# Kernel optimization log

Measured on AMD Instinct MI355X. Metric: run time of the kernel, lower is better.

## Reference

```python
import jax, jax.numpy as jnp
import numpy as np

B, T, P, K, R, M = 32, 2048, 128, 256, 8, 64
TAU, TAU_X, TAU_Z = 5, 100.0, 100.0


def _mlp(x, layers):
    # torch nn.Linear: y = x @ W.T + b, each followed by tanh
    for W, b in layers:
        x = jnp.tanh(x @ W.T + b)
    return x


def setup_inputs() -> dict:
    key = jax.random.key(0)
    ks = jax.random.split(key, 24)
    g = lambda k, shp, s=0.1: (jax.random.normal(k, shp, dtype=jnp.float32) * s)
    inp = {
        "in_seq": jax.random.normal(ks[0], (B, T, P), dtype=jnp.float32),
        "L": g(ks[1], (K, R)),
        "Rm": g(ks[2], (K, R)),
        "Wz": g(ks[3], (M, M)),
        "Az_w": g(ks[4], (R, M)),
        "Az_b": jnp.zeros((R,), jnp.float32),
        "ex1_w": g(ks[5], (K, P)), "ex1_b": jnp.zeros((K,), jnp.float32),
        "ex2_w": g(ks[6], (K, K)), "ex2_b": jnp.zeros((K,), jnp.float32),
        "ex3_w": g(ks[7], (K, K)), "ex3_b": jnp.zeros((K,), jnp.float32),
        "ez1_w": g(ks[8], (M, P)), "ez1_b": jnp.zeros((M,), jnp.float32),
        "ez2_w": g(ks[9], (M, M)), "ez2_b": jnp.zeros((M,), jnp.float32),
        "ez3_w": g(ks[10], (M, M)), "ez3_b": jnp.zeros((M,), jnp.float32),
        "de1_w": g(ks[11], (K, K)), "de1_b": jnp.zeros((K,), jnp.float32),
        "de2_w": g(ks[12], (P, K)), "de2_b": jnp.zeros((P,), jnp.float32),
    }
    return inp


def reference(in_seq, L, Rm, Wz, Az_w, Az_b,
              ex1_w, ex1_b, ex2_w, ex2_b, ex3_w, ex3_b,
              ez1_w, ez1_b, ez2_w, ez2_b, ez3_w, ez3_b,
              de1_w, de1_b, de2_w, de2_b):
    enc_x = [(ex1_w, ex1_b), (ex2_w, ex2_b), (ex3_w, ex3_b)]
    enc_z = [(ez1_w, ez1_b), (ez2_w, ez2_b), (ez3_w, ez3_b)]
    dec = [(de1_w, de1_b), (de2_w, de2_b)]

    x_seq = _mlp(in_seq, enc_x)  # [B,T,K]
    z_seq = _mlp(in_seq, enc_z)  # [B,T,M]

    def step(carry, inp):
        x, z = carry          # [B,K], [B,M]
        t, xt, zt = inp       # scalar, [B,K], [B,M]
        # teacher forcing reset every TAU steps (not at t=0)
        reset = (t % TAU == 0) & (t > 0)
        x = jnp.where(reset, xt, x)
        z = jnp.where(reset, zt, z)
        # neuromodulator dynamics
        dz = -z + jnp.tanh(z) @ Wz.T
        z = z + dz / TAU_Z
        s = jax.nn.sigmoid(z @ Az_w.T + Az_b)  # [B,R]
        # low-rank recurrence: bmm(tanh(x), einsum('bir,jr,kr->bijk',s,L,R)[:,0])
        # == ((tanh(x) @ L) * s) @ R.T   (same math, O(K*R) per element)
        dx = -x + ((jnp.tanh(x) @ L) * s) @ Rm.T
        x = x + dx / TAU_X
        x_dec = _mlp(x, dec)  # [B,P]
        return (x, z), (x_dec, z)

    x0 = x_seq[:, 0, :]
    z0 = z_seq[:, 0, :]
    ts = jnp.arange(T)
    xs = jnp.swapaxes(x_seq, 0, 1)  # [T,B,K]
    zs = jnp.swapaxes(z_seq, 0, 1)  # [T,B,M]
    _, (x_pred_t, z_pred_t) = jax.lax.scan(step, (x0, z0), (ts, xs, zs))
    x_pred = jnp.swapaxes(x_pred_t, 0, 1)  # [B,T,P]
    z_pred = jnp.swapaxes(z_pred_t, 0, 1)  # [B,T,M]

    x_recon = _mlp(x_seq, dec)  # [B,T,P]
    return (x_pred, x_recon, z_pred, z_seq)
```

## Files before the change

kernel.cpp:

```cpp
#include <hip/hip_runtime.h>
#include <math.h>

constexpr int B = 32, T = 2048, P = 128, K = 256, R = 8, M = 64;
constexpr int BT = B * T;
constexpr int TAU = 5;
constexpr int NSEG = (T + TAU - 1) / TAU;
constexpr float INV_TAU_X = 1.0f / 100.0f;
constexpr float INV_TAU_Z = 1.0f / 100.0f;

typedef short bf16x4 __attribute__((ext_vector_type(4)));
typedef short bf16x8 __attribute__((ext_vector_type(8)));
typedef float f32x4 __attribute__((ext_vector_type(4)));

static __device__ __forceinline__ short f2bf(float f) {
  unsigned u = __builtin_bit_cast(unsigned, f);
  u += 0x7FFF + ((u >> 16) & 1);
  return (short)(u >> 16);
}
static __device__ __forceinline__ float bf2f(short h) {
  unsigned u = ((unsigned)(unsigned short)h) << 16;
  return __builtin_bit_cast(float, u);
}

static __device__ __forceinline__ float tanh_fast(float x) {
  const float e = __expf(2.f * x);
  return 1.f - 2.f * __builtin_amdgcn_rcpf(e + 1.f);
}
static __device__ __forceinline__ float sigmoid_fast(float x) {
  return __builtin_amdgcn_rcpf(1.f + __expf(-x));
}

template <int CTRL>
static __device__ __forceinline__ float dppadd(float p) {
  return p + __builtin_bit_cast(
                 float, __builtin_amdgcn_update_dpp(
                            0, __builtin_bit_cast(int, p), CTRL, 0xF, 0xF, true));
}

static __device__ __forceinline__ void allreduce8(float p[R]) {
#pragma unroll
  for (int r = 0; r < R; ++r) p[r] = dppadd<0xB1>(p[r]);
#pragma unroll
  for (int r = 0; r < R; ++r) p[r] = dppadd<0x4E>(p[r]);
#pragma unroll
  for (int r = 0; r < R; ++r) p[r] = dppadd<0x141>(p[r]);
#pragma unroll
  for (int r = 0; r < R; ++r) p[r] = dppadd<0x140>(p[r]);
#pragma unroll
  for (int r = 0; r < R; ++r)
    p[r] += __builtin_bit_cast(float, __builtin_amdgcn_ds_swizzle(
                                          __builtin_bit_cast(int, p[r]), 0x401F));
#pragma unroll
  for (int r = 0; r < R; ++r)
    p[r] += __shfl_xor(p[r], 32, 64);
}

struct W8 {
  const float* src[8];
  unsigned hoff[8];
  unsigned n4[8];
};
__global__ __launch_bounds__(256) void split8_kernel(W8 p, short* __restrict__ dst) {
  const int w = blockIdx.y;
  const int i = blockIdx.x * 256 + threadIdx.x;
  if (i >= (int)p.n4[w]) return;
  const float4 v = ((const float4*)p.src[w])[i];
  const float f[4] = {v.x, v.y, v.z, v.w};
  bf16x4 ph, pl;
#pragma unroll
  for (int q = 0; q < 4; ++q) {
    ph[q] = f2bf(f[q]);
    pl[q] = f2bf(f[q] - bf2f(ph[q]));
  }
  *(bf16x4*)&dst[p.hoff[w] + i * 4] = ph;
  *(bf16x4*)&dst[p.hoff[w] + p.n4[w] * 4 + i * 4] = pl;
}

struct FusedArgs {
  const float* A0;
  const short* Wh[5];
  const short* Wl[5];
  const float* bias[5];
  float* gout[5];
};

template <int I> struct Ly { static constexpr int v = I; };

template <int MAXW, int NL, int K0, int K1, int K2, int K3, int K4, int K5>
__global__ __launch_bounds__(512, 4) void fused_mlp(FusedArgs p) {
  constexpr int Kd[6] = {K0, K1, K2, K3, K4, K5};
  __shared__ short bufh[64 * MAXW];
  __shared__ short bufl[64 * MAXW];

  const int tid = threadIdx.x;
  const int wave = tid >> 6, lane = tid & 63;
  const int l16 = lane & 15, quad = lane >> 4;
  const int wm = wave >> 2, cg = wave & 3;
  const int row0 = blockIdx.x * 64;

  constexpr int G0 = K0 / 8;
  for (int u = tid; u < 64 * G0; u += 512) {
    const int row = u / G0, g = u % G0;
    const float* gp = p.A0 + (size_t)(row0 + row) * K0 + g * 8;
    const f32x4 v0 = *(const f32x4*)gp;
    const f32x4 v1 = *(const f32x4*)(gp + 4);
    bf16x8 ph, pl;
#pragma unroll
    for (int e = 0; e < 4; ++e) {
      ph[e] = f2bf(v0[e]);
      pl[e] = f2bf(v0[e] - bf2f(ph[e]));
      ph[4 + e] = f2bf(v1[e]);
      pl[4 + e] = f2bf(v1[e] - bf2f(ph[4 + e]));
    }
    const int off = ((g >> 3) * 64 + row) * 64 + (((g & 7) ^ (row & 7)) * 8);
    *(bf16x8*)&bufh[off] = ph;
    *(bf16x8*)&bufl[off] = pl;
  }
  __syncthreads();

  auto do_layer = [&](auto lc) {
    constexpr int l = decltype(lc)::v;
    constexpr int KIN = Kd[l], KOUT = Kd[l + 1];
    constexpr int JT = KOUT / 64;
    constexpr int NT64 = KIN / 64;
    const int cols0w = cg * (KOUT / 4);

    f32x4 acc[2][JT];
#pragma unroll
    for (int i = 0; i < 2; ++i)
#pragma unroll
      for (int j = 0; j < JT; ++j) acc[i][j] = (f32x4){0.f, 0.f, 0.f, 0.f};

#pragma unroll
    for (int kt = 0; kt < NT64; ++kt) {
#pragma unroll
      for (int kk = 0; kk < 2; ++kk) {
        const int qc = kk * 4 + quad;
        bf16x8 bh[JT], bl[JT];
#pragma unroll
        for (int j = 0; j < JT; ++j) {
          const size_t boff = (size_t)(cols0w + j * 16 + l16) * KIN +
                              kt * 64 + kk * 32 + quad * 8;
          bh[j] = *(const bf16x8*)(p.Wh[l] + boff);
          bl[j] = *(const bf16x8*)(p.Wl[l] + boff);
        }
        bf16x8 ah[2], al[2];
#pragma unroll
        for (int i = 0; i < 2; ++i) {
          const int r = wm * 32 + i * 16 + l16;
          const int off = (kt * 64 + r) * 64 + ((qc ^ (r & 7)) * 8);
          ah[i] = *(const bf16x8*)&bufh[off];
          al[i] = *(const bf16x8*)&bufl[off];
        }
#pragma unroll
        for (int j = 0; j < JT; ++j)
#pragma unroll
          for (int i = 0; i < 2; ++i) {
            acc[i][j] = __builtin_amdgcn_mfma_f32_16x16x32_bf16(
                ah[i], bh[j], acc[i][j], 0, 0, 0);
            acc[i][j] = __builtin_amdgcn_mfma_f32_16x16x32_bf16(
                al[i], bh[j], acc[i][j], 0, 0, 0);
            acc[i][j] = __builtin_amdgcn_mfma_f32_16x16x32_bf16(
                ah[i], bl[j], acc[i][j], 0, 0, 0);
          }
      }
    }
    if constexpr (l < NL - 1) __syncthreads();

    float* gout = p.gout[l];
#pragma unroll
    for (int j = 0; j < JT; ++j) {
      const int col = cols0w + j * 16 + l16;
      const float bj = p.bias[l][col];
#pragma unroll
      for (int i = 0; i < 2; ++i) {
#pragma unroll
        for (int r = 0; r < 4; ++r) {
          const float v = tanh_fast(acc[i][j][r] + bj);
          const int row = wm * 32 + i * 16 + quad * 4 + r;
          if constexpr (l < NL - 1) {
            const int off = ((col >> 6) * 64 + row) * 64 +
                            ((((col & 63) >> 3) ^ (row & 7)) * 8) + (col & 7);
            const short h = f2bf(v);
            bufh[off] = h;
            bufl[off] = f2bf(v - bf2f(h));
          }
          if (gout) gout[(size_t)(row0 + row) * KOUT + col] = v;
        }
      }
    }
    if constexpr (l < NL - 1) __syncthreads();
  };

  do_layer(Ly<0>{});
  if constexpr (NL > 1) do_layer(Ly<1>{});
  if constexpr (NL > 2) do_layer(Ly<2>{});
  if constexpr (NL > 3) do_layer(Ly<3>{});
  if constexpr (NL > 4) do_layer(Ly<4>{});
}

__global__ __launch_bounds__(512) void scan_kernel(
    float* xs,
    const float* __restrict__ z_seq,
    const float* __restrict__ Lm, const float* __restrict__ Rm,
    const float* __restrict__ Wz, const float* __restrict__ Az_w,
    const float* __restrict__ Az_b,
    float* __restrict__ z_pred) {
  __shared__ __align__(16) float Wz_s[M][68];
  __shared__ __align__(16) float Ls[K * R];
  __shared__ __align__(16) float Rs[K * R];
  __shared__ __align__(16) float tz_s[8][M];

  const int tid = threadIdx.x;
  for (int i = tid; i < M * M; i += 512) Wz_s[i >> 6][i & 63] = Wz[i];
  ((float4*)Ls)[tid] = ((const float4*)Lm)[tid];
  ((float4*)Rs)[tid] = ((const float4*)Rm)[tid];
  __syncthreads();

  const int wave = tid >> 6;
  const int lane = tid & 63;
  const int chain = blockIdx.x * 8 + wave;
  const int b = chain / NSEG;
  const int seg = chain % NSEG;
  const int t0 = seg * TAU;

  float azw[R], azb[R];
#pragma unroll
  for (int r = 0; r < R; ++r) {
    azw[r] = Az_w[r * M + lane];
    azb[r] = Az_b[r];
  }

  float x[4], z;
  {
    const size_t base = ((size_t)b * T + t0);
#pragma unroll
    for (int j = 0; j < 4; ++j) x[j] = xs[base * K + lane + 64 * j];
    z = z_seq[base * M + lane];
  }

  const float4* wrow = (const float4*)&Wz_s[lane][0];
  const float4* trow = (const float4*)&tz_s[wave][0];

  for (int tt = 0; tt < TAU; ++tt) {
    const int t = t0 + tt;
    const float tz = tanh_fast(z);
    tz_s[wave][lane] = tz;
    float zacc = 0.f;
#pragma unroll
    for (int j = 0; j < 16; ++j) {
      const float4 w = wrow[j], tv = trow[j];
      zacc += w.x * tv.x + w.y * tv.y + w.z * tv.z + w.w * tv.w;
    }
    const float znew = z + (zacc - z) * INV_TAU_Z;

    float s[R];
#pragma unroll
    for (int r = 0; r < R; ++r) s[r] = znew * azw[r];
    allreduce8(s);
#pragma unroll
    for (int r = 0; r < R; ++r) s[r] = sigmoid_fast(s[r] + azb[r]);

    float tx4[4];
#pragma unroll
    for (int j = 0; j < 4; ++j) tx4[j] = tanh_fast(x[j]);
    float v[R];
#pragma unroll
    for (int r = 0; r < R; ++r) v[r] = 0.f;
#pragma unroll
    for (int j = 0; j < 4; ++j) {
      const int kb = (lane + 64 * j) * 8;
      const f32x4 la = *(const f32x4*)&Ls[kb];
      const f32x4 lb = *(const f32x4*)&Ls[kb + 4];
      const float txj = tx4[j];
      v[0] += txj * la[0]; v[1] += txj * la[1];
      v[2] += txj * la[2]; v[3] += txj * la[3];
      v[4] += txj * lb[0]; v[5] += txj * lb[1];
      v[6] += txj * lb[2]; v[7] += txj * lb[3];
    }
    allreduce8(v);
#pragma unroll
    for (int r = 0; r < R; ++r) v[r] *= s[r];
#pragma unroll
    for (int j = 0; j < 4; ++j) {
      const int kb = (lane + 64 * j) * 8;
      const f32x4 ra = *(const f32x4*)&Rs[kb];
      const f32x4 rb = *(const f32x4*)&Rs[kb + 4];
      const float xacc = v[0] * ra[0] + v[1] * ra[1] + v[2] * ra[2] +
                         v[3] * ra[3] + v[4] * rb[0] + v[5] * rb[1] +
                         v[6] * rb[2] + v[7] * rb[3];
      x[j] = x[j] + (xacc - x[j]) * INV_TAU_X;
    }

    if (t < T) {
      const size_t o = ((size_t)b * T + t);
#pragma unroll
      for (int j = 0; j < 4; ++j) xs[o * K + lane + 64 * j] = x[j];
      z_pred[o * M + lane] = znew;
    }
    z = znew;
  }
}

extern "C" void kernel_launch(void* const* d_in, const int* in_sizes, int n_in,
                              void* d_out, int out_size, void* d_ws,
                              size_t ws_size, hipStream_t stream) {
  const float* in_seq = (const float*)d_in[0];
  const float* Lm    = (const float*)d_in[1];
  const float* Rm    = (const float*)d_in[2];
  const float* Wz    = (const float*)d_in[3];
  const float* Az_w  = (const float*)d_in[4];
  const float* Az_b  = (const float*)d_in[5];
  const float* ex1_w = (const float*)d_in[6];
  const float* ex1_b = (const float*)d_in[7];
  const float* ex2_w = (const float*)d_in[8];
  const float* ex2_b = (const float*)d_in[9];
  const float* ex3_w = (const float*)d_in[10];
  const float* ex3_b = (const float*)d_in[11];
  const float* ez1_w = (const float*)d_in[12];
  const float* ez1_b = (const float*)d_in[13];
  const float* ez2_w = (const float*)d_in[14];
  const float* ez2_b = (const float*)d_in[15];
  const float* ez3_w = (const float*)d_in[16];
  const float* ez3_b = (const float*)d_in[17];
  const float* de1_w = (const float*)d_in[18];
  const float* de1_b = (const float*)d_in[19];
  const float* de2_w = (const float*)d_in[20];
  const float* de2_b = (const float*)d_in[21];

  float* out = (float*)d_out;
  float* x_pred  = out;
  float* x_recon = out + (size_t)BT * P;
  float* z_pred  = out + (size_t)2 * BT * P;
  float* z_seq   = out + (size_t)2 * BT * P + (size_t)BT * M;

  float* X0 = (float*)d_ws;
  short* Wr = (short*)(X0 + (size_t)BT * K);

  const unsigned HO_EX1 = 0,      HO_EX2 = 65536,  HO_EX3 = 196608;
  const unsigned HO_DE1 = 327680, HO_DE2 = 458752;
  const unsigned HO_EZ1 = 524288, HO_EZ2 = 540672, HO_EZ3 = 548864;

  W8 w8;
  w8.src[0] = ex1_w; w8.hoff[0] = HO_EX1; w8.n4[0] = 8192;
  w8.src[1] = ex2_w; w8.hoff[1] = HO_EX2; w8.n4[1] = 16384;
  w8.src[2] = ex3_w; w8.hoff[2] = HO_EX3; w8.n4[2] = 16384;
  w8.src[3] = de1_w; w8.hoff[3] = HO_DE1; w8.n4[3] = 16384;
  w8.src[4] = de2_w; w8.hoff[4] = HO_DE2; w8.n4[4] = 8192;
  w8.src[5] = ez1_w; w8.hoff[5] = HO_EZ1; w8.n4[5] = 2048;
  w8.src[6] = ez2_w; w8.hoff[6] = HO_EZ2; w8.n4[6] = 1024;
  w8.src[7] = ez3_w; w8.hoff[7] = HO_EZ3; w8.n4[7] = 1024;
  split8_kernel<<<dim3(64, 8), dim3(256), 0, stream>>>(w8, Wr);

  const dim3 fgrid(BT / 64), fblk(512);

  {
    FusedArgs a{};
    a.A0 = in_seq;
    a.Wh[0] = Wr + HO_EX1; a.Wl[0] = Wr + HO_EX1 + 32768; a.bias[0] = ex1_b;
    a.Wh[1] = Wr + HO_EX2; a.Wl[1] = Wr + HO_EX2 + 65536; a.bias[1] = ex2_b;
    a.Wh[2] = Wr + HO_EX3; a.Wl[2] = Wr + HO_EX3 + 65536; a.bias[2] = ex3_b;
    a.Wh[3] = Wr + HO_DE1; a.Wl[3] = Wr + HO_DE1 + 65536; a.bias[3] = de1_b;
    a.Wh[4] = Wr + HO_DE2; a.Wl[4] = Wr + HO_DE2 + 32768; a.bias[4] = de2_b;
    a.gout[2] = X0;
    a.gout[4] = x_recon;
    fused_mlp<256, 5, 128, 256, 256, 256, 256, 128>
        <<<fgrid, fblk, 0, stream>>>(a);
  }
  {
    FusedArgs a{};
    a.A0 = in_seq;
    a.Wh[0] = Wr + HO_EZ1; a.Wl[0] = Wr + HO_EZ1 + 8192; a.bias[0] = ez1_b;
    a.Wh[1] = Wr + HO_EZ2; a.Wl[1] = Wr + HO_EZ2 + 4096; a.bias[1] = ez2_b;
    a.Wh[2] = Wr + HO_EZ3; a.Wl[2] = Wr + HO_EZ3 + 4096; a.bias[2] = ez3_b;
    a.gout[2] = z_seq;
    fused_mlp<128, 3, 128, 64, 64, 64, 0, 0><<<fgrid, fblk, 0, stream>>>(a);
  }
  scan_kernel<<<dim3(B * NSEG / 8), dim3(512), 0, stream>>>(
      X0, z_seq, Lm, Rm, Wz, Az_w, Az_b, z_pred);
  {
    FusedArgs a{};
    a.A0 = X0;
    a.Wh[0] = Wr + HO_DE1; a.Wl[0] = Wr + HO_DE1 + 65536; a.bias[0] = de1_b;
    a.Wh[1] = Wr + HO_DE2; a.Wl[1] = Wr + HO_DE2 + 32768; a.bias[1] = de2_b;
    a.gout[1] = x_pred;
    fused_mlp<256, 2, 256, 256, 128, 0, 0, 0><<<fgrid, fblk, 0, stream>>>(a);
  }
}
```

Measured before the change: 618.8 us.

## Reshape fused MLP wave tiling per layer and prefetch weight fragments three deep

The fused MLP kernel now picks its wave layout per layer: 8 column groups by 1 row group when the output width is at least 128, otherwise 4 by 2. Each wave then owns more rows (up to 64) or fewer columns, which changes how much each global weight fragment is reused. Weight fragments also go into a three-slot register ring that is loaded two k-phases ahead of use, so global-load latency is hidden behind the MFMAs. The cost is more register pressure, since the ring and the larger accumulator sets may cause spills under launch_bounds(512,4), and narrow layers get less column parallelism.

```diff
diff --git a/kernel.cpp b/kernel.cpp
--- a/kernel.cpp
+++ b/kernel.cpp
@@ -95,7 +95,6 @@
   const int tid = threadIdx.x;
   const int wave = tid >> 6, lane = tid & 63;
   const int l16 = lane & 15, quad = lane >> 4;
-  const int wm = wave >> 2, cg = wave & 3;
   const int row0 = blockIdx.x * 64;
 
   constexpr int G0 = K0 / 8;
@@ -121,49 +120,59 @@
   auto do_layer = [&](auto lc) {
     constexpr int l = decltype(lc)::v;
     constexpr int KIN = Kd[l], KOUT = Kd[l + 1];
-    constexpr int JT = KOUT / 64;
-    constexpr int NT64 = KIN / 64;
-    const int cols0w = cg * (KOUT / 4);
-
-    f32x4 acc[2][JT];
-#pragma unroll
-    for (int i = 0; i < 2; ++i)
+    constexpr int NWN = (KOUT >= 128) ? 8 : 4;
+    constexpr int NWM = 8 / NWN;
+    constexpr int NI = 4 / NWM;
+    constexpr int JT = KOUT / (NWN * 16);
+    constexpr int NPH = KIN / 32;
+    const int wm = wave / NWN, cg = wave % NWN;
+    const int cols0w = cg * (KOUT / NWN);
+    const int rbase = wm * NI * 16;
+
+    f32x4 acc[NI][JT];
+#pragma unroll
+    for (int i = 0; i < NI; ++i)
 #pragma unroll
       for (int j = 0; j < JT; ++j) acc[i][j] = (f32x4){0.f, 0.f, 0.f, 0.f};
 
-#pragma unroll
-    for (int kt = 0; kt < NT64; ++kt) {
-#pragma unroll
-      for (int kk = 0; kk < 2; ++kk) {
-        const int qc = kk * 4 + quad;
-        bf16x8 bh[JT], bl[JT];
-#pragma unroll
-        for (int j = 0; j < JT; ++j) {
-          const size_t boff = (size_t)(cols0w + j * 16 + l16) * KIN +
-                              kt * 64 + kk * 32 + quad * 8;
-          bh[j] = *(const bf16x8*)(p.Wh[l] + boff);
-          bl[j] = *(const bf16x8*)(p.Wl[l] + boff);
+    bf16x8 bh[3][JT], bl[3][JT];
+    auto loadB = [&](int ph, int slot) {
+#pragma unroll
+      for (int j = 0; j < JT; ++j) {
+        const size_t boff =
+            (size_t)(cols0w + j * 16 + l16) * KIN + ph * 32 + quad * 8;
+        bh[slot][j] = *(const bf16x8*)(p.Wh[l] + boff);
+        bl[slot][j] = *(const bf16x8*)(p.Wl[l] + boff);
+      }
+    };
+    loadB(0, 0);
+    if constexpr (NPH > 1) loadB(1, 1);
+
+#pragma unroll
+    for (int ph = 0; ph < NPH; ++ph) {
+      if (ph + 2 < NPH) loadB(ph + 2, (ph + 2) % 3);
+      const int kt = ph >> 1;
+      const int qc = (ph & 1) * 4 + quad;
+      bf16x8 ah[NI], al[NI];
+#pragma unroll
+      for (int i = 0; i < NI; ++i) {
+        const int r = rbase + i * 16 + l16;
+        const int off = (kt * 64 + r) * 64 + ((qc ^ (r & 7)) * 8);
+        ah[i] = *(const bf16x8*)&bufh[off];
+        al[i] = *(const bf16x8*)&bufl[off];
+      }
+      const int s = ph % 3;
+#pragma unroll
+      for (int j = 0; j < JT; ++j)
+#pragma unroll
+        for (int i = 0; i < NI; ++i) {
+          acc[i][j] = __builtin_amdgcn_mfma_f32_16x16x32_bf16(
+              ah[i], bh[s][j], acc[i][j], 0, 0, 0);
+          acc[i][j] = __builtin_amdgcn_mfma_f32_16x16x32_bf16(
+              al[i], bh[s][j], acc[i][j], 0, 0, 0);
+          acc[i][j] = __builtin_amdgcn_mfma_f32_16x16x32_bf16(
+              ah[i], bl[s][j], acc[i][j], 0, 0, 0);
         }
-        bf16x8 ah[2], al[2];
-#pragma unroll
-        for (int i = 0; i < 2; ++i) {
-          const int r = wm * 32 + i * 16 + l16;
-          const int off = (kt * 64 + r) * 64 + ((qc ^ (r & 7)) * 8);
-          ah[i] = *(const bf16x8*)&bufh[off];
-          al[i] = *(const bf16x8*)&bufl[off];
-        }
-#pragma unroll
-        for (int j = 0; j < JT; ++j)
-#pragma unroll
-          for (int i = 0; i < 2; ++i) {
-            acc[i][j] = __builtin_amdgcn_mfma_f32_16x16x32_bf16(
-                ah[i], bh[j], acc[i][j], 0, 0, 0);
-            acc[i][j] = __builtin_amdgcn_mfma_f32_16x16x32_bf16(
-                al[i], bh[j], acc[i][j], 0, 0, 0);
-            acc[i][j] = __builtin_amdgcn_mfma_f32_16x16x32_bf16(
-                ah[i], bl[j], acc[i][j], 0, 0, 0);
-          }
-      }
     }
     if constexpr (l < NL - 1) __syncthreads();
 
@@ -173,11 +182,11 @@
       const int col = cols0w + j * 16 + l16;
       const float bj = p.bias[l][col];
 #pragma unroll
-      for (int i = 0; i < 2; ++i) {
+      for (int i = 0; i < NI; ++i) {
 #pragma unroll
         for (int r = 0; r < 4; ++r) {
           const float v = tanh_fast(acc[i][j][r] + bj);
-          const int row = wm * 32 + i * 16 + quad * 4 + r;
+          const int row = rbase + i * 16 + quad * 4 + r;
           if constexpr (l < NL - 1) {
             const int off = ((col >> 6) * 64 + row) * 64 +
                             ((((col & 63) >> 3) ^ (row & 7)) * 8) + (col & 7);
```

Result: faster. 520.8 us (-15.8%).
